# Kernel tuning notes

Measured on AMD Instinct MI355X. Metric: run time of the kernel, lower is better.

## Reference

```python
import jax, jax.numpy as jnp
import numpy as np

# Static problem structure (matches setup_inputs)
B, NPOLY, VPP, L = 32, 256, 64, 32
LAYERS = 3
PLEN = L * 2 ** LAYERS  # 256
LN_EPS = 1e-5


def _layernorm(h, g, b):
    mu = h.mean(-1, keepdims=True)
    var = ((h - mu) ** 2).mean(-1, keepdims=True)
    return g * (h - mu) / jnp.sqrt(var + LN_EPS) + b


def _forward(data, W0, b0, g0, beta0, W1, b1, g1, beta1, W2, b2, g2, beta2,
             Wq, bq, Wk, bk, Wv, bv):
    # row 0 holds agent polyline index in feature 0
    agent_id = data[:, 0, 0].astype(jnp.int32)  # [B]
    vecs = data[:, 1:, :]
    vecs = vecs.at[:, :, -1].set(0.0)  # zero out polyline-id feature (data[:,:,-1]=0)
    x = vecs.reshape(B, NPOLY, VPP, L)  # uniform polyline groups

    # SubGraph: 3 layers of (MLP -> maxpool aggregate -> concat), doubling width
    for (W, b, g, be) in ((W0, b0, g0, beta0), (W1, b1, g1, beta1), (W2, b2, g2, beta2)):
        h = jax.nn.relu(_layernorm(x @ W + b, g, be))  # [B,P,V,c]
        agg = h.max(axis=2, keepdims=True)             # [B,P,1,c]
        x = jnp.concatenate([h, jnp.broadcast_to(agg, h.shape)], axis=-1)  # [B,P,V,2c]
    P = x.max(axis=2)  # [B, NPOLY, PLEN] polyline features

    # Global graph: single-head attention with agent polyline as query
    q = P[jnp.arange(B), agent_id] @ Wq + bq          # [B, C]
    k = P @ Wk + bk                                    # [B, P, C]
    v = P @ Wv + bv
    scores = jnp.einsum('bc,bpc->bp', q, k) / jnp.sqrt(jnp.float32(PLEN))
    att = jax.nn.softmax(scores, axis=-1)
    return jnp.einsum('bp,bpc->bc', att, v)           # [B, PLEN]


def setup_inputs() -> dict:
    key = jax.random.key(0)
    ks = jax.random.split(key, 24)
    V = 1 + NPOLY * VPP
    data = jax.random.normal(ks[0], (B, V, L), dtype=jnp.float32)
    agent = jax.random.randint(ks[1], (B,), 0, NPOLY).astype(jnp.float32)
    data = data.at[:, 0, :].set(0.0).at[:, 0, 0].set(agent)
    pid = jnp.repeat(jnp.arange(NPOLY), VPP).astype(jnp.float32)
    data = data.at[:, 1:, -1].set(pid[None, :])

    inp = {'data': data}
    c = L
    for i in range(LAYERS):
        inp[f'W{i}'] = 0.02 * jax.random.normal(ks[2 + i], (c, c), dtype=jnp.float32)
        inp[f'b{i}'] = jnp.zeros((c,), jnp.float32)
        inp[f'g{i}'] = jnp.ones((c,), jnp.float32)
        inp[f'beta{i}'] = jnp.zeros((c,), jnp.float32)
        c *= 2
    C = PLEN
    for j, nm in enumerate(('q', 'k', 'v')):
        inp[f'W{nm}'] = 0.02 * jax.random.normal(ks[10 + j], (C, C), dtype=jnp.float32)
        inp[f'b{nm}'] = jnp.zeros((C,), jnp.float32)
    return inp


def reference(data, W0, b0, g0, beta0, W1, b1, g1, beta1, W2, b2, g2, beta2,
              Wq, bq, Wk, bk, Wv, bv):
    return _forward(data, W0, b0, g0, beta0, W1, b1, g1, beta1, W2, b2, g2, beta2,
                    Wq, bq, Wk, bk, Wv, bv)
```

## Files before the change

### kernel.cpp

```cpp
#include <hip/hip_runtime.h>

#define NPOLY 256
#define VPP   64
#define LCH   32
#define NV    (1 + NPOLY * VPP)
#define LN_EPS 1e-5f

typedef __bf16 bf16x8 __attribute__((ext_vector_type(8)));
typedef float  f32x4  __attribute__((ext_vector_type(4)));

union U4B8 { uint4 u; bf16x8 v; };

__device__ __forceinline__ unsigned f2bf_u(float f) {
    unsigned u = __float_as_uint(f);
    return (u + 0x7FFFu + ((u >> 16) & 1u)) >> 16;
}
__device__ __forceinline__ unsigned packbf(float a, float b) {
    return f2bf_u(a) | (f2bf_u(b) << 16);
}

__global__ void vn_prep1(const float* __restrict__ W0, const float* __restrict__ W1,
                         const float* __restrict__ W2,
                         const float* __restrict__ Wq, const float* __restrict__ Wk,
                         const float* __restrict__ Wv,
                         float* __restrict__ Wqf, float* __restrict__ Wkf,
                         float* __restrict__ Wvf, uint4* __restrict__ wpack)
{
    int t = blockIdx.x * 256 + threadIdx.x;
    if (t < 3 * 32768) {
        int which = t >> 15, r = t & 32767;
        const float* src = which == 0 ? Wq : which == 1 ? Wk : Wv;
        float*       dst = which == 0 ? Wqf : which == 1 ? Wkf : Wvf;
        dst[r] = src[r] + src[r + 128 * 256];
        return;
    }
    t -= 3 * 32768;
    if (t >= 22 * 64) return;
    int f = t >> 6, L = t & 63, q = L >> 4, m = L & 15;
    const float* src; int N, k0, col;
    if (f < 2)      { src = W0; N = 32;  k0 = q * 8;                 col = f * 16 + m; }
    else if (f < 6) { src = W1; N = 64;  k0 = q * 8;                 col = (f - 2) * 16 + m; }
    else { int g = f - 6; src = W2; N = 128; k0 = (g >> 3) * 32 + q * 8; col = (g & 7) * 16 + m; }
    float e[8];
    #pragma unroll
    for (int j = 0; j < 8; j++) e[j] = src[(k0 + j) * N + col];
    uint4 o;
    o.x = packbf(e[0], e[1]); o.y = packbf(e[2], e[3]);
    o.z = packbf(e[4], e[5]); o.w = packbf(e[6], e[7]);
    wpack[f * 64 + L] = o;
}

__global__ void vn_prep2(const float* __restrict__ Wqf, const float* __restrict__ Wkf,
                         const float* __restrict__ bq,
                         float* __restrict__ Mff, float* __restrict__ u0f)
{
    int t = blockIdx.x * 256 + threadIdx.x;
    if (t < 16384) {
        int i = t >> 7, j = t & 127;
        const float* a = Wqf + i * 256;
        const float* b = Wkf + j * 256;
        float s = 0.f;
        for (int c = 0; c < 256; c++) s = fmaf(a[c], b[c], s);
        Mff[i * 128 + j] = s;
    } else if (t < 16512) {
        int j = t - 16384;
        const float* b = Wkf + j * 256;
        float s = 0.f;
        for (int c = 0; c < 256; c++) s = fmaf(bq[c], b[c], s);
        u0f[j] = s;
    }
}

__global__ __launch_bounds__(64, 2) void vn_mlp(
    const float* __restrict__ data, const uint4* __restrict__ wpack,
    const float* __restrict__ b0, const float* __restrict__ g0, const float* __restrict__ be0,
    const float* __restrict__ W1, const float* __restrict__ b1,
    const float* __restrict__ g1, const float* __restrict__ be1,
    const float* __restrict__ W2, const float* __restrict__ b2,
    const float* __restrict__ g2, const float* __restrict__ be2,
    float* __restrict__ Ph)
{
    __shared__ __align__(16) unsigned short hbuf[64 * 72];
    __shared__ float fbuf[192];

    const int blk = blockIdx.x;
    const int L = threadIdx.x, q = L >> 4, m = L & 15;
    const int bb = blk >> 8, pp = blk & 255;

    const float* rowbase = data + ((size_t)bb * NV + 1 + (size_t)pp * VPP) * LCH;
    bf16x8 A0[4];
    #pragma unroll
    for (int rt = 0; rt < 4; rt++) {
        const float* rp = rowbase + (size_t)(rt * 16 + m) * LCH + q * 8;
        float4 u = *(const float4*)rp;
        float4 v = *(const float4*)(rp + 4);
        if (q == 3) v.w = 0.f;
        U4B8 c;
        c.u.x = packbf(u.x, u.y); c.u.y = packbf(u.z, u.w);
        c.u.z = packbf(v.x, v.y); c.u.w = packbf(v.z, v.w);
        A0[rt] = c.v;
    }
    U4B8 t0, t1; t0.u = wpack[0 * 64 + L]; t1.u = wpack[1 * 64 + L];
    float bc0[2] = { b0[m], b0[16 + m] };
    f32x4 acc0[4][2];
    #pragma unroll
    for (int rt = 0; rt < 4; rt++) {
        {
            f32x4 a = { bc0[0], bc0[0], bc0[0], bc0[0] };
            acc0[rt][0] = __builtin_amdgcn_mfma_f32_16x16x32_bf16(A0[rt], t0.v, a, 0, 0, 0);
        }
        {
            f32x4 a = { bc0[1], bc0[1], bc0[1], bc0[1] };
            acc0[rt][1] = __builtin_amdgcn_mfma_f32_16x16x32_bf16(A0[rt], t1.v, a, 0, 0, 0);
        }
    }
    float g0c[2]  = { g0[m],  g0[16 + m]  };
    float be0c[2] = { be0[m], be0[16 + m] };
    float a0mx[2] = { 0.f, 0.f };
    #pragma unroll
    for (int rt = 0; rt < 4; rt++) {
        #pragma unroll
        for (int reg = 0; reg < 4; reg++) {
            float x0 = acc0[rt][0][reg], x1 = acc0[rt][1][reg];
            float rs = x0 + x1, rq = x0 * x0 + x1 * x1;
            #pragma unroll
            for (int s = 1; s < 16; s <<= 1) { rs += __shfl_xor(rs, s, 64); rq += __shfl_xor(rq, s, 64); }
            float mu = rs * (1.f / 32.f);
            float var = rq * (1.f / 32.f) - mu * mu;
            float ri = rsqrtf(var + LN_EPS);
            #pragma unroll
            for (int ct = 0; ct < 2; ct++) {
                float v = fmaxf(fmaf(g0c[ct] * ri, acc0[rt][ct][reg] - mu, be0c[ct]), 0.f);
                acc0[rt][ct][reg] = v;
                a0mx[ct] = fmaxf(a0mx[ct], v);
            }
        }
    }
    #pragma unroll
    for (int ct = 0; ct < 2; ct++) {
        float v = a0mx[ct];
        v = fmaxf(v, __shfl_xor(v, 16, 64));
        v = fmaxf(v, __shfl_xor(v, 32, 64));
        a0mx[ct] = v;
    }
    if (q == 0) { fbuf[m] = a0mx[0]; fbuf[16 + m] = a0mx[1]; }
    __syncthreads();
    float au1 = b1[L];
    for (int j = 0; j < 32; j++)
        au1 = fmaf(fbuf[j], W1[(32 + j) * 64 + L], au1);
    #pragma unroll
    for (int rt = 0; rt < 4; rt++)
        #pragma unroll
        for (int reg = 0; reg < 4; reg++) {
            int row = rt * 16 + q * 4 + reg;
            hbuf[row * 72 + m]      = (unsigned short)f2bf_u(acc0[rt][0][reg]);
            hbuf[row * 72 + 16 + m] = (unsigned short)f2bf_u(acc0[rt][1][reg]);
        }
    __syncthreads();
    fbuf[64 + L] = au1;
    __syncthreads();

    bf16x8 A1[4];
    #pragma unroll
    for (int rt = 0; rt < 4; rt++) {
        U4B8 c; c.u = *(const uint4*)(hbuf + (rt * 16 + m) * 72 + q * 8);
        A1[rt] = c.v;
    }
    f32x4 acc1[4][4];
    #pragma unroll
    for (int ct = 0; ct < 4; ct++) {
        U4B8 w; w.u = wpack[(2 + ct) * 64 + L];
        float au = fbuf[64 + ct * 16 + m];
        #pragma unroll
        for (int rt = 0; rt < 4; rt++) {
            f32x4 a = { au, au, au, au };
            acc1[rt][ct] = __builtin_amdgcn_mfma_f32_16x16x32_bf16(A1[rt], w.v, a, 0, 0, 0);
        }
    }
    float g1c[4], be1c[4];
    #pragma unroll
    for (int ct = 0; ct < 4; ct++) { g1c[ct] = g1[ct * 16 + m]; be1c[ct] = be1[ct * 16 + m]; }
    float a1mx[4] = { 0.f, 0.f, 0.f, 0.f };
    #pragma unroll
    for (int rt = 0; rt < 4; rt++) {
        #pragma unroll
        for (int reg = 0; reg < 4; reg++) {
            float rs = 0.f, rq = 0.f;
            #pragma unroll
            for (int ct = 0; ct < 4; ct++) { float x = acc1[rt][ct][reg]; rs += x; rq += x * x; }
            #pragma unroll
            for (int s = 1; s < 16; s <<= 1) { rs += __shfl_xor(rs, s, 64); rq += __shfl_xor(rq, s, 64); }
            float mu = rs * (1.f / 64.f);
            float var = rq * (1.f / 64.f) - mu * mu;
            float ri = rsqrtf(var + LN_EPS);
            #pragma unroll
            for (int ct = 0; ct < 4; ct++) {
                float v = fmaxf(fmaf(g1c[ct] * ri, acc1[rt][ct][reg] - mu, be1c[ct]), 0.f);
                acc1[rt][ct][reg] = v;
                a1mx[ct] = fmaxf(a1mx[ct], v);
            }
        }
    }
    #pragma unroll
    for (int ct = 0; ct < 4; ct++) {
        float v = a1mx[ct];
        v = fmaxf(v, __shfl_xor(v, 16, 64));
        v = fmaxf(v, __shfl_xor(v, 32, 64));
        a1mx[ct] = v;
    }
    __syncthreads();
    if (q == 0) {
        #pragma unroll
        for (int ct = 0; ct < 4; ct++) fbuf[ct * 16 + m] = a1mx[ct];
    }
    __syncthreads();
    float au2a = b2[L], au2b = b2[64 + L];
    for (int j = 0; j < 64; j++) {
        float av = fbuf[j];
        au2a = fmaf(av, W2[(64 + j) * 128 + L],      au2a);
        au2b = fmaf(av, W2[(64 + j) * 128 + 64 + L], au2b);
    }
    #pragma unroll
    for (int rt = 0; rt < 4; rt++)
        #pragma unroll
        for (int reg = 0; reg < 4; reg++) {
            int row = rt * 16 + q * 4 + reg;
            #pragma unroll
            for (int ct = 0; ct < 4; ct++)
                hbuf[row * 72 + ct * 16 + m] = (unsigned short)f2bf_u(acc1[rt][ct][reg]);
        }
    __syncthreads();
    fbuf[64 + L] = au2a; fbuf[128 + L] = au2b;
    __syncthreads();

    bf16x8 A2[4][2];
    #pragma unroll
    for (int rt = 0; rt < 4; rt++)
        #pragma unroll
        for (int ks = 0; ks < 2; ks++) {
            U4B8 c; c.u = *(const uint4*)(hbuf + (rt * 16 + m) * 72 + ks * 32 + q * 8);
            A2[rt][ks] = c.v;
        }
    f32x4 acc2[8][4];
    #pragma unroll
    for (int ct = 0; ct < 8; ct++) {
        U4B8 wa, wb;
        wa.u = wpack[(6 + ct) * 64 + L];
        wb.u = wpack[(14 + ct) * 64 + L];
        float au = fbuf[64 + ct * 16 + m];
        #pragma unroll
        for (int rt = 0; rt < 4; rt++) {
            f32x4 a = { au, au, au, au };
            a = __builtin_amdgcn_mfma_f32_16x16x32_bf16(A2[rt][0], wa.v, a, 0, 0, 0);
            a = __builtin_amdgcn_mfma_f32_16x16x32_bf16(A2[rt][1], wb.v, a, 0, 0, 0);
            acc2[ct][rt] = a;
        }
    }
    float g2c[8], be2c[8];
    #pragma unroll
    for (int ct = 0; ct < 8; ct++) { g2c[ct] = g2[ct * 16 + m]; be2c[ct] = be2[ct * 16 + m]; }
    float m2[8] = { 0.f, 0.f, 0.f, 0.f, 0.f, 0.f, 0.f, 0.f };
    #pragma unroll
    for (int rt = 0; rt < 4; rt++) {
        #pragma unroll
        for (int reg = 0; reg < 4; reg++) {
            float rs = 0.f, rq = 0.f;
            #pragma unroll
            for (int ct = 0; ct < 8; ct++) { float x = acc2[ct][rt][reg]; rs += x; rq += x * x; }
            #pragma unroll
            for (int s = 1; s < 16; s <<= 1) { rs += __shfl_xor(rs, s, 64); rq += __shfl_xor(rq, s, 64); }
            float mu = rs * (1.f / 128.f);
            float var = rq * (1.f / 128.f) - mu * mu;
            float ri = rsqrtf(var + LN_EPS);
            #pragma unroll
            for (int ct = 0; ct < 8; ct++) {
                float v = fmaxf(fmaf(g2c[ct] * ri, acc2[ct][rt][reg] - mu, be2c[ct]), 0.f);
                m2[ct] = fmaxf(m2[ct], v);
            }
        }
    }
    #pragma unroll
    for (int ct = 0; ct < 8; ct++) {
        float v = m2[ct];
        v = fmaxf(v, __shfl_xor(v, 16, 64));
        v = fmaxf(v, __shfl_xor(v, 32, 64));
        m2[ct] = v;
    }
    float v1 = q == 0 ? m2[0] : q == 1 ? m2[1] : q == 2 ? m2[2] : m2[3];
    float v2 = q == 0 ? m2[4] : q == 1 ? m2[5] : q == 2 ? m2[6] : m2[7];
    float* op = Ph + (size_t)blk * 128;
    op[L] = v1; op[64 + L] = v2;
}

__global__ __launch_bounds__(256) void vn_attn(
    const float* __restrict__ data, const float* __restrict__ Ph,
    const float* __restrict__ Mff, const float* __restrict__ u0f,
    const float* __restrict__ Wvf, const float* __restrict__ bv,
    float* __restrict__ out)
{
    __shared__ float pah[128], tts[128], sc[256], pb[128], red[8];
    const int b = blockIdx.x, tid = threadIdx.x, lane = tid & 63, wave = tid >> 6;
    const float* PhB = Ph + (size_t)b * NPOLY * 128;
    const int agent = (int)data[(size_t)b * NV * LCH];

    if (tid < 128) pah[tid] = PhB[(size_t)agent * 128 + tid];
    __syncthreads();
    if (tid < 128) {
        float a = u0f[tid];
        for (int i = 0; i < 128; i++) a = fmaf(pah[i], Mff[i * 128 + tid], a);
        tts[tid] = a;
    }
    __syncthreads();
    for (int pi = 0; pi < 64; pi++) {
        const int p = wave * 64 + pi;
        const float* pr = PhB + (size_t)p * 128;
        float s = pr[lane] * tts[lane];
        s = fmaf(pr[64 + lane], tts[64 + lane], s);
        #pragma unroll
        for (int st = 1; st < 64; st <<= 1) s += __shfl_xor(s, st, 64);
        if (lane == 0) sc[p] = s * 0.0625f;
    }
    __syncthreads();
    float sv = sc[tid];
    float mx = sv;
    #pragma unroll
    for (int s = 1; s < 64; s <<= 1) mx = fmaxf(mx, __shfl_xor(mx, s, 64));
    if (lane == 0) red[wave] = mx;
    __syncthreads();
    mx = fmaxf(fmaxf(red[0], red[1]), fmaxf(red[2], red[3]));
    float e = expf(sv - mx);
    float sm = e;
    #pragma unroll
    for (int s = 1; s < 64; s <<= 1) sm += __shfl_xor(sm, s, 64);
    if (lane == 0) red[4 + wave] = sm;
    __syncthreads();
    const float tot = red[4] + red[5] + red[6] + red[7];
    sc[tid] = e / tot;
    __syncthreads();
    if (tid < 128) {
        float a = 0.f;
        for (int p = 0; p < 256; p++) a = fmaf(sc[p], PhB[(size_t)p * 128 + tid], a);
        pb[tid] = a;
    }
    __syncthreads();
    float o = bv[tid];
    for (int j = 0; j < 128; j++) o = fmaf(pb[j], Wvf[j * 256 + tid], o);
    out[(size_t)b * 256 + tid] = o;
}

extern "C" void kernel_launch(void* const* d_in, const int* in_sizes, int n_in,
                              void* d_out, int out_size, void* d_ws, size_t ws_size,
                              hipStream_t stream)
{
    const float* data = (const float*)d_in[0];
    const float* W0 = (const float*)d_in[1];
    const float* b0 = (const float*)d_in[2];
    const float* g0 = (const float*)d_in[3];
    const float* be0= (const float*)d_in[4];
    const float* W1 = (const float*)d_in[5];
    const float* b1 = (const float*)d_in[6];
    const float* g1 = (const float*)d_in[7];
    const float* be1= (const float*)d_in[8];
    const float* W2 = (const float*)d_in[9];
    const float* b2 = (const float*)d_in[10];
    const float* g2 = (const float*)d_in[11];
    const float* be2= (const float*)d_in[12];
    const float* Wq = (const float*)d_in[13];
    const float* bq = (const float*)d_in[14];
    const float* Wk = (const float*)d_in[15];
    const float* bk = (const float*)d_in[16];
    const float* Wv = (const float*)d_in[17];
    const float* bv = (const float*)d_in[18];
    (void)bk;

    char* wsb = (char*)d_ws;
    float* Ph    = (float*)(wsb);
    float* Wqf   = (float*)(wsb + 4194304);
    float* Wkf   = (float*)(wsb + 4325376);
    float* Wvf   = (float*)(wsb + 4456448);
    float* Mff   = (float*)(wsb + 4587520);
    float* u0f   = (float*)(wsb + 4653056);
    uint4* wpack = (uint4*)(wsb + 4653568);

    vn_prep1<<<390, 256, 0, stream>>>(W0, W1, W2, Wq, Wk, Wv, Wqf, Wkf, Wvf, wpack);
    vn_prep2<<<65, 256, 0, stream>>>(Wqf, Wkf, bq, Mff, u0f);
    vn_mlp<<<32 * NPOLY, 64, 0, stream>>>(data, wpack,
                                          b0, g0, be0,
                                          W1, b1, g1, be1,
                                          W2, b2, g2, be2, Ph);
    vn_attn<<<32, 256, 0, stream>>>(data, Ph, Mff, u0f, Wvf, bv, (float*)d_out);
}
```

Before: 235.0 us.

## Pack four polylines per MLP block, use hardware bf16 convert, restructure attention

The MLP kernel now runs four independent 64-thread polyline workers per 256-thread block, each with its own shared-memory slice, and uses wave barriers instead of block-wide syncthreads. Float-to-bf16 packing switches from manual integer rounding to the v_cvt_pk_bf16_f32 instruction. The attention kernel spreads the tts, score, weighted-sum and output-projection loops across all 256 threads with split accumulators and vectorized loads, and the prep kernel uses float4 dot products. The aim is to cut launch and sync overhead and raise parallelism in the serial attention phase. The cost is higher per-block register and LDS pressure, and a possible change in bf16 rounding behaviour.

```diff
diff --git a/kernel.cpp b/kernel.cpp
--- a/kernel.cpp
+++ b/kernel.cpp
@@ -11,12 +11,10 @@
 
 union U4B8 { uint4 u; bf16x8 v; };
 
-__device__ __forceinline__ unsigned f2bf_u(float f) {
-    unsigned u = __float_as_uint(f);
-    return (u + 0x7FFFu + ((u >> 16) & 1u)) >> 16;
-}
 __device__ __forceinline__ unsigned packbf(float a, float b) {
-    return f2bf_u(a) | (f2bf_u(b) << 16);
+    unsigned r;
+    asm("v_cvt_pk_bf16_f32 %0, %1, %2" : "=v"(r) : "v"(a), "v"(b));
+    return r;
 }
 
 __global__ void vn_prep1(const float* __restrict__ W0, const float* __restrict__ W1,
@@ -57,21 +55,32 @@
     int t = blockIdx.x * 256 + threadIdx.x;
     if (t < 16384) {
         int i = t >> 7, j = t & 127;
-        const float* a = Wqf + i * 256;
-        const float* b = Wkf + j * 256;
-        float s = 0.f;
-        for (int c = 0; c < 256; c++) s = fmaf(a[c], b[c], s);
-        Mff[i * 128 + j] = s;
+        const float4* a = (const float4*)(Wqf + i * 256);
+        const float4* b = (const float4*)(Wkf + j * 256);
+        float s0 = 0.f, s1 = 0.f, s2 = 0.f, s3 = 0.f;
+        #pragma unroll 4
+        for (int c = 0; c < 64; c++) {
+            float4 A = a[c], B = b[c];
+            s0 = fmaf(A.x, B.x, s0); s1 = fmaf(A.y, B.y, s1);
+            s2 = fmaf(A.z, B.z, s2); s3 = fmaf(A.w, B.w, s3);
+        }
+        Mff[i * 128 + j] = (s0 + s1) + (s2 + s3);
     } else if (t < 16512) {
         int j = t - 16384;
-        const float* b = Wkf + j * 256;
-        float s = 0.f;
-        for (int c = 0; c < 256; c++) s = fmaf(bq[c], b[c], s);
-        u0f[j] = s;
-    }
-}
-
-__global__ __launch_bounds__(64, 2) void vn_mlp(
+        const float4* a = (const float4*)bq;
+        const float4* b = (const float4*)(Wkf + j * 256);
+        float s0 = 0.f, s1 = 0.f, s2 = 0.f, s3 = 0.f;
+        #pragma unroll 4
+        for (int c = 0; c < 64; c++) {
+            float4 A = a[c], B = b[c];
+            s0 = fmaf(A.x, B.x, s0); s1 = fmaf(A.y, B.y, s1);
+            s2 = fmaf(A.z, B.z, s2); s3 = fmaf(A.w, B.w, s3);
+        }
+        u0f[j] = (s0 + s1) + (s2 + s3);
+    }
+}
+
+__global__ __launch_bounds__(256, 4) void vn_mlp(
     const float* __restrict__ data, const uint4* __restrict__ wpack,
     const float* __restrict__ b0, const float* __restrict__ g0, const float* __restrict__ be0,
     const float* __restrict__ W1, const float* __restrict__ b1,
@@ -80,12 +89,15 @@
     const float* __restrict__ g2, const float* __restrict__ be2,
     float* __restrict__ Ph)
 {
-    __shared__ __align__(16) unsigned short hbuf[64 * 72];
-    __shared__ float fbuf[192];
-
-    const int blk = blockIdx.x;
-    const int L = threadIdx.x, q = L >> 4, m = L & 15;
+    __shared__ __align__(16) unsigned short hbuf[4][64 * 72];
+    __shared__ float fbuf[4][192];
+
+    const int w = threadIdx.x >> 6;
+    const int L = threadIdx.x & 63, q = L >> 4, m = L & 15;
+    const int blk = blockIdx.x * 4 + w;
     const int bb = blk >> 8, pp = blk & 255;
+    unsigned short* hb = hbuf[w];
+    float* fb = fbuf[w];
 
     const float* rowbase = data + ((size_t)bb * NV + 1 + (size_t)pp * VPP) * LCH;
     bf16x8 A0[4];
@@ -143,38 +155,42 @@
         v = fmaxf(v, __shfl_xor(v, 32, 64));
         a0mx[ct] = v;
     }
-    if (q == 0) { fbuf[m] = a0mx[0]; fbuf[16 + m] = a0mx[1]; }
-    __syncthreads();
-    float au1 = b1[L];
-    for (int j = 0; j < 32; j++)
-        au1 = fmaf(fbuf[j], W1[(32 + j) * 64 + L], au1);
+    if (q == 0) { fb[m] = a0mx[0]; fb[16 + m] = a0mx[1]; }
+    __builtin_amdgcn_wave_barrier();
+    float au1a = b1[L], au1b = 0.f;
+    for (int j = 0; j < 32; j += 2) {
+        au1a = fmaf(fb[j],     W1[(32 + j) * 64 + L],     au1a);
+        au1b = fmaf(fb[j + 1], W1[(32 + j + 1) * 64 + L], au1b);
+    }
+    float au1 = au1a + au1b;
     #pragma unroll
     for (int rt = 0; rt < 4; rt++)
         #pragma unroll
         for (int reg = 0; reg < 4; reg++) {
             int row = rt * 16 + q * 4 + reg;
-            hbuf[row * 72 + m]      = (unsigned short)f2bf_u(acc0[rt][0][reg]);
-            hbuf[row * 72 + 16 + m] = (unsigned short)f2bf_u(acc0[rt][1][reg]);
-        }
-    __syncthreads();
-    fbuf[64 + L] = au1;
-    __syncthreads();
+            unsigned u = packbf(acc0[rt][0][reg], acc0[rt][1][reg]);
+            hb[row * 72 + m]      = (unsigned short)u;
+            hb[row * 72 + 16 + m] = (unsigned short)(u >> 16);
+        }
+    __builtin_amdgcn_wave_barrier();
+    fb[64 + L] = au1;
+    __builtin_amdgcn_wave_barrier();
 
     bf16x8 A1[4];
     #pragma unroll
     for (int rt = 0; rt < 4; rt++) {
-        U4B8 c; c.u = *(const uint4*)(hbuf + (rt * 16 + m) * 72 + q * 8);
+        U4B8 c; c.u = *(const uint4*)(hb + (rt * 16 + m) * 72 + q * 8);
         A1[rt] = c.v;
     }
     f32x4 acc1[4][4];
     #pragma unroll
     for (int ct = 0; ct < 4; ct++) {
-        U4B8 w; w.u = wpack[(2 + ct) * 64 + L];
-        float au = fbuf[64 + ct * 16 + m];
+        U4B8 wv; wv.u = wpack[(2 + ct) * 64 + L];
+        float au = fb[64 + ct * 16 + m];
         #pragma unroll
         for (int rt = 0; rt < 4; rt++) {
             f32x4 a = { au, au, au, au };
-            acc1[rt][ct] = __builtin_amdgcn_mfma_f32_16x16x32_bf16(A1[rt], w.v, a, 0, 0, 0);
+            acc1[rt][ct] = __builtin_amdgcn_mfma_f32_16x16x32_bf16(A1[rt], wv.v, a, 0, 0, 0);
         }
     }
     float g1c[4], be1c[4];
@@ -208,37 +224,43 @@
         v = fmaxf(v, __shfl_xor(v, 32, 64));
         a1mx[ct] = v;
     }
-    __syncthreads();
+    __builtin_amdgcn_wave_barrier();
     if (q == 0) {
         #pragma unroll
-        for (int ct = 0; ct < 4; ct++) fbuf[ct * 16 + m] = a1mx[ct];
-    }
-    __syncthreads();
-    float au2a = b2[L], au2b = b2[64 + L];
-    for (int j = 0; j < 64; j++) {
-        float av = fbuf[j];
-        au2a = fmaf(av, W2[(64 + j) * 128 + L],      au2a);
-        au2b = fmaf(av, W2[(64 + j) * 128 + 64 + L], au2b);
-    }
+        for (int ct = 0; ct < 4; ct++) fb[ct * 16 + m] = a1mx[ct];
+    }
+    __builtin_amdgcn_wave_barrier();
+    float au2a = b2[L], au2b = b2[64 + L], au2c = 0.f, au2d = 0.f;
+    for (int j = 0; j < 64; j += 2) {
+        float av0 = fb[j], av1 = fb[j + 1];
+        au2a = fmaf(av0, W2[(64 + j) * 128 + L],          au2a);
+        au2b = fmaf(av0, W2[(64 + j) * 128 + 64 + L],     au2b);
+        au2c = fmaf(av1, W2[(64 + j + 1) * 128 + L],      au2c);
+        au2d = fmaf(av1, W2[(64 + j + 1) * 128 + 64 + L], au2d);
+    }
+    au2a += au2c; au2b += au2d;
     #pragma unroll
     for (int rt = 0; rt < 4; rt++)
         #pragma unroll
         for (int reg = 0; reg < 4; reg++) {
             int row = rt * 16 + q * 4 + reg;
-            #pragma unroll
-            for (int ct = 0; ct < 4; ct++)
-                hbuf[row * 72 + ct * 16 + m] = (unsigned short)f2bf_u(acc1[rt][ct][reg]);
-        }
-    __syncthreads();
-    fbuf[64 + L] = au2a; fbuf[128 + L] = au2b;
-    __syncthreads();
+            unsigned ua = packbf(acc1[rt][0][reg], acc1[rt][1][reg]);
+            unsigned ub = packbf(acc1[rt][2][reg], acc1[rt][3][reg]);
+            hb[row * 72 + m]      = (unsigned short)ua;
+            hb[row * 72 + 16 + m] = (unsigned short)(ua >> 16);
+            hb[row * 72 + 32 + m] = (unsigned short)ub;
+            hb[row * 72 + 48 + m] = (unsigned short)(ub >> 16);
+        }
+    __builtin_amdgcn_wave_barrier();
+    fb[64 + L] = au2a; fb[128 + L] = au2b;
+    __builtin_amdgcn_wave_barrier();
 
     bf16x8 A2[4][2];
     #pragma unroll
     for (int rt = 0; rt < 4; rt++)
         #pragma unroll
         for (int ks = 0; ks < 2; ks++) {
-            U4B8 c; c.u = *(const uint4*)(hbuf + (rt * 16 + m) * 72 + ks * 32 + q * 8);
+            U4B8 c; c.u = *(const uint4*)(hb + (rt * 16 + m) * 72 + ks * 32 + q * 8);
             A2[rt][ks] = c.v;
         }
     f32x4 acc2[8][4];
@@ -247,7 +269,7 @@
         U4B8 wa, wb;
         wa.u = wpack[(6 + ct) * 64 + L];
         wb.u = wpack[(14 + ct) * 64 + L];
-        float au = fbuf[64 + ct * 16 + m];
+        float au = fb[64 + ct * 16 + m];
         #pragma unroll
         for (int rt = 0; rt < 4; rt++) {
             f32x4 a = { au, au, au, au };
@@ -298,30 +320,53 @@
     const float* __restrict__ Wvf, const float* __restrict__ bv,
     float* __restrict__ out)
 {
-    __shared__ float pah[128], tts[128], sc[256], pb[128], red[8];
+    __shared__ __align__(16) float pah[128], tts[128], att[256], pb[128];
+    __shared__ __align__(16) float part[256];
+    __shared__ float red[8];
     const int b = blockIdx.x, tid = threadIdx.x, lane = tid & 63, wave = tid >> 6;
     const float* PhB = Ph + (size_t)b * NPOLY * 128;
     const int agent = (int)data[(size_t)b * NV * LCH];
 
     if (tid < 128) pah[tid] = PhB[(size_t)agent * 128 + tid];
     __syncthreads();
-    if (tid < 128) {
-        float a = u0f[tid];
-        for (int i = 0; i < 128; i++) a = fmaf(pah[i], Mff[i * 128 + tid], a);
-        tts[tid] = a;
-    }
-    __syncthreads();
-    for (int pi = 0; pi < 64; pi++) {
-        const int p = wave * 64 + pi;
-        const float* pr = PhB + (size_t)p * 128;
-        float s = pr[lane] * tts[lane];
-        s = fmaf(pr[64 + lane], tts[64 + lane], s);
-        #pragma unroll
-        for (int st = 1; st < 64; st <<= 1) s += __shfl_xor(s, st, 64);
-        if (lane == 0) sc[p] = s * 0.0625f;
-    }
-    __syncthreads();
-    float sv = sc[tid];
+
+    {
+        const int j = tid & 127, h = tid >> 7;
+        const float* mc = Mff + (size_t)(h * 64) * 128 + j;
+        const float* pv = pah + h * 64;
+        float s0 = 0.f, s1 = 0.f, s2 = 0.f, s3 = 0.f;
+        for (int i = 0; i < 64; i += 4) {
+            s0 = fmaf(pv[i],     mc[(i)     * 128], s0);
+            s1 = fmaf(pv[i + 1], mc[(i + 1) * 128], s1);
+            s2 = fmaf(pv[i + 2], mc[(i + 2) * 128], s2);
+            s3 = fmaf(pv[i + 3], mc[(i + 3) * 128], s3);
+        }
+        part[tid] = (s0 + s1) + (s2 + s3);
+    }
+    __syncthreads();
+    if (tid < 128) tts[tid] = part[tid] + part[128 + tid] + u0f[tid];
+    __syncthreads();
+
+    float sv;
+    {
+        const float* pr = PhB + (size_t)tid * 128;
+        float s0 = 0.f, s1 = 0.f, s2 = 0.f, s3 = 0.f;
+        for (int j = 0; j < 128; j += 16) {
+            float4 x0 = *(const float4*)(pr + j);
+            float4 x1 = *(const float4*)(pr + j + 4);
+            float4 x2 = *(const float4*)(pr + j + 8);
+            float4 x3 = *(const float4*)(pr + j + 12);
+            float4 t0 = *(const float4*)(tts + j);
+            float4 t1 = *(const float4*)(tts + j + 4);
+            float4 t2 = *(const float4*)(tts + j + 8);
+            float4 t3 = *(const float4*)(tts + j + 12);
+            s0 = fmaf(x0.w, t0.w, fmaf(x0.z, t0.z, fmaf(x0.y, t0.y, fmaf(x0.x, t0.x, s0))));
+            s1 = fmaf(x1.w, t1.w, fmaf(x1.z, t1.z, fmaf(x1.y, t1.y, fmaf(x1.x, t1.x, s1))));
+            s2 = fmaf(x2.w, t2.w, fmaf(x2.z, t2.z, fmaf(x2.y, t2.y, fmaf(x2.x, t2.x, s2))));
+            s3 = fmaf(x3.w, t3.w, fmaf(x3.z, t3.z, fmaf(x3.y, t3.y, fmaf(x3.x, t3.x, s3))));
+        }
+        sv = ((s0 + s1) + (s2 + s3)) * 0.0625f;
+    }
     float mx = sv;
     #pragma unroll
     for (int s = 1; s < 64; s <<= 1) mx = fmaxf(mx, __shfl_xor(mx, s, 64));
@@ -335,17 +380,37 @@
     if (lane == 0) red[4 + wave] = sm;
     __syncthreads();
     const float tot = red[4] + red[5] + red[6] + red[7];
-    sc[tid] = e / tot;
-    __syncthreads();
-    if (tid < 128) {
-        float a = 0.f;
-        for (int p = 0; p < 256; p++) a = fmaf(sc[p], PhB[(size_t)p * 128 + tid], a);
-        pb[tid] = a;
-    }
-    __syncthreads();
-    float o = bv[tid];
-    for (int j = 0; j < 128; j++) o = fmaf(pb[j], Wvf[j * 256 + tid], o);
-    out[(size_t)b * 256 + tid] = o;
+    att[tid] = e / tot;
+    __syncthreads();
+
+    {
+        const int c = tid & 127, h = tid >> 7;
+        const float* pp = PhB + (size_t)(h * 128) * 128 + c;
+        const float* ap = att + h * 128;
+        float s0 = 0.f, s1 = 0.f, s2 = 0.f, s3 = 0.f;
+        for (int p = 0; p < 128; p += 4) {
+            s0 = fmaf(ap[p],     pp[(p)     * 128], s0);
+            s1 = fmaf(ap[p + 1], pp[(p + 1) * 128], s1);
+            s2 = fmaf(ap[p + 2], pp[(p + 2) * 128], s2);
+            s3 = fmaf(ap[p + 3], pp[(p + 3) * 128], s3);
+        }
+        part[tid] = (s0 + s1) + (s2 + s3);
+    }
+    __syncthreads();
+    if (tid < 128) pb[tid] = part[tid] + part[128 + tid];
+    __syncthreads();
+
+    {
+        const float* wv = Wvf + tid;
+        float s0 = 0.f, s1 = 0.f, s2 = 0.f, s3 = 0.f;
+        for (int j = 0; j < 128; j += 4) {
+            s0 = fmaf(pb[j],     wv[(j)     * 256], s0);
+            s1 = fmaf(pb[j + 1], wv[(j + 1) * 256], s1);
+            s2 = fmaf(pb[j + 2], wv[(j + 2) * 256], s2);
+            s3 = fmaf(pb[j + 3], wv[(j + 3) * 256], s3);
+        }
+        out[(size_t)b * 256 + tid] = bv[tid] + ((s0 + s1) + (s2 + s3));
+    }
 }
 
 extern "C" void kernel_launch(void* const* d_in, const int* in_sizes, int n_in,
@@ -384,9 +449,9 @@
 
     vn_prep1<<<390, 256, 0, stream>>>(W0, W1, W2, Wq, Wk, Wv, Wqf, Wkf, Wvf, wpack);
     vn_prep2<<<65, 256, 0, stream>>>(Wqf, Wkf, bq, Mff, u0f);
-    vn_mlp<<<32 * NPOLY, 64, 0, stream>>>(data, wpack,
-                                          b0, g0, be0,
-                                          W1, b1, g1, be1,
-                                          W2, b2, g2, be2, Ph);
+    vn_mlp<<<32 * NPOLY / 4, 256, 0, stream>>>(data, wpack,
+                                               b0, g0, be0,
+                                               W1, b1, g1, be1,
+                                               W2, b2, g2, be2, Ph);
     vn_attn<<<32, 256, 0, stream>>>(data, Ph, Mff, u0f, Wvf, bv, (float*)d_out);
 }
```

After: 252.5 us. 1.07x slower.
